# Kernel tuning notes

Measured on AMD Instinct MI355X. Metric: run time of the kernel, lower is better.

Reference implementation:

```python
import jax, jax.numpy as jnp
import numpy as np
from jax import lax

B = 16384
D_MODEL = 84
N_EXPERTS = 2
TOP_K = 2
HIDDEN = 2048


def _conv(x, w, b):
    # x: [N,C,H,W], w: [O,I,kh,kw] (torch OIHW), VALID padding, stride 1
    y = lax.conv_general_dilated(x, w, (1, 1), 'VALID',
                                 dimension_numbers=('NCHW', 'OIHW', 'NCHW'))
    return y + b[None, :, None, None]


def _maxpool2(x):
    return lax.reduce_window(x, -jnp.inf, lax.max,
                             (1, 1, 2, 2), (1, 1, 2, 2), 'VALID')


def setup_inputs() -> dict:
    key = jax.random.key(0)
    ks = jax.random.split(key, 17)
    s = 0.05
    return {
        'x': jax.random.normal(ks[0], (B, 3, 32, 32), jnp.float32),
        'conv1_w': jax.random.normal(ks[1], (6, 3, 5, 5), jnp.float32) * s,
        'conv1_b': jax.random.normal(ks[2], (6,), jnp.float32) * s,
        'conv2_w': jax.random.normal(ks[3], (16, 6, 5, 5), jnp.float32) * s,
        'conv2_b': jax.random.normal(ks[4], (16,), jnp.float32) * s,
        'fc1_w': jax.random.normal(ks[5], (400, 120), jnp.float32) * s,
        'fc1_b': jax.random.normal(ks[6], (120,), jnp.float32) * s,
        'fc2_w': jax.random.normal(ks[7], (120, 84), jnp.float32) * s,
        'fc2_b': jax.random.normal(ks[8], (84,), jnp.float32) * s,
        'gate_w': jax.random.normal(ks[9], (D_MODEL, N_EXPERTS), jnp.float32) * s,
        'exp_w1': jax.random.normal(ks[10], (N_EXPERTS, D_MODEL, HIDDEN), jnp.float32) * s,
        'exp_b1': jax.random.normal(ks[11], (N_EXPERTS, HIDDEN), jnp.float32) * s,
        'exp_w2': jax.random.normal(ks[12], (N_EXPERTS, HIDDEN, D_MODEL), jnp.float32) * s,
        'exp_b2': jax.random.normal(ks[13], (N_EXPERTS, D_MODEL), jnp.float32) * s,
        'fc3_w': jax.random.normal(ks[14], (84, 10), jnp.float32) * s,
        'fc3_b': jax.random.normal(ks[15], (10,), jnp.float32) * s,
    }


def _moe(x, gate_w, exp_w1, exp_b1, exp_w2, exp_b2):
    # tutel top-k gate: softmax over expert logits, select top-k, renormalize
    n = x.shape[0]
    scores = jax.nn.softmax(x @ gate_w, axis=-1)          # [N,E]
    top_v, top_i = lax.top_k(scores, TOP_K)               # [N,k]
    gates = top_v / jnp.sum(top_v, axis=-1, keepdims=True)
    # dense combine weights [N,E] (zero where not routed)
    comb = jnp.zeros((n, N_EXPERTS), x.dtype).at[
        jnp.arange(n)[:, None], top_i].set(gates)
    # grouped expert FFN (E=2: evaluate both, weight-combine)
    h = jax.nn.relu(jnp.einsum('nd,edh->enh', x, exp_w1) + exp_b1[:, None, :])
    y = jnp.einsum('enh,ehd->end', h, exp_w2) + exp_b2[:, None, :]  # [E,N,D]
    return jnp.einsum('ne,end->nd', comb, y)


def reference(x, conv1_w, conv1_b, conv2_w, conv2_b, fc1_w, fc1_b,
              fc2_w, fc2_b, gate_w, exp_w1, exp_b1, exp_w2, exp_b2,
              fc3_w, fc3_b):
    h = _maxpool2(jax.nn.relu(_conv(x, conv1_w, conv1_b)))   # [B,6,14,14]
    h = _maxpool2(jax.nn.relu(_conv(h, conv2_w, conv2_b)))   # [B,16,5,5]
    h = h.reshape(-1, 16 * 5 * 5)                            # [B,400]
    h = jax.nn.relu(h @ fc1_w + fc1_b)                       # [B,120]
    h = jax.nn.relu(h @ fc2_w + fc2_b)                       # [B,84]
    h = _moe(h, gate_w, exp_w1, exp_b1, exp_w2, exp_b2)      # [B,84]
    return h @ fc3_w + fc3_b                                 # [B,10]
```

## Files before the change

kernel.cpp:

```cpp
#include <hip/hip_runtime.h>
#include <stdint.h>

typedef unsigned short u16;
typedef __attribute__((ext_vector_type(8))) short s8v;
typedef __attribute__((ext_vector_type(4))) float f4v;
typedef __fp16 h2v __attribute__((ext_vector_type(2)));
typedef __fp16 h8v __attribute__((ext_vector_type(8)));

__device__ __forceinline__ float bu2f(u16 u) {
  return __uint_as_float(((uint32_t)u) << 16);
}
__device__ __forceinline__ u16 f2bu(float f) {
  uint32_t u = __float_as_uint(f);
  u += 0x7fffu + ((u >> 16) & 1u);
  return (u16)(u >> 16);
}

union U32H2 { uint32_t u; h2v h; };

__device__ __forceinline__ uint32_t pk2h(float a, float b) {
  U32H2 x;
  x.h = __builtin_amdgcn_cvt_pkrtz(a, b);
  return x.u;
}

template <bool F32> struct In;
template <> struct In<true> {
  static __device__ __forceinline__ float ld(const void* p, long i) {
    return ((const float*)p)[i];
  }
};
template <> struct In<false> {
  static __device__ __forceinline__ float ld(const void* p, long i) {
    return bu2f(((const u16*)p)[i]);
  }
};

__global__ void k_detect(const u16* __restrict__ x, int* __restrict__ flag) {
  __shared__ int s[64];
  int cnt = 0;
  for (int i = threadIdx.x; i < 2048; i += 64) {
    int e = (x[i] >> 7) & 0xFF;
    cnt += (e >= 96 && e <= 134) ? 1 : 0;
  }
  s[threadIdx.x] = cnt;
  __syncthreads();
  if (threadIdx.x == 0) {
    int t = 0;
    for (int i = 0; i < 64; ++i) t += s[i];
    *flag = (t >= 1843) ? 0 : 1;
  }
}

__device__ __forceinline__ u16 f2h16(float f) {
  __fp16 h = (__fp16)f;
  u16 r;
  __builtin_memcpy(&r, &h, 2);
  return r;
}

template <bool INF32>
__global__ __launch_bounds__(256) void k_trans(
    const int* __restrict__ flag,
    const void* __restrict__ fc1w, const void* __restrict__ fc2w,
    const void* __restrict__ ew1, const void* __restrict__ ew2,
    const void* __restrict__ c1w, const void* __restrict__ c1b,
    const void* __restrict__ c2w, const void* __restrict__ c2b,
    u16* __restrict__ fc1t, u16* __restrict__ fc2t,
    u16* __restrict__ w1t, u16* __restrict__ w2t,
    uint32_t* __restrict__ cdw) {
  if (*flag != (INF32 ? 1 : 0)) return;
  long gid = (long)blockIdx.x * 256 + threadIdx.x;
  if (gid < 53248) {
    int n = (int)(gid / 416), k = (int)(gid % 416);
    fc1t[gid] = (n < 120 && k < 400) ? f2bu(In<INF32>::ld(fc1w, (long)k * 120 + n)) : (u16)0;
  } else if (gid < 65536) {
    long i = gid - 53248;
    int n = (int)(i / 128), k = (int)(i % 128);
    fc2t[i] = (n < 84 && k < 120) ? f2bu(In<INF32>::ld(fc2w, (long)k * 84 + n)) : (u16)0;
  } else if (gid < 458752) {
    long i = gid - 65536;
    int e = (int)(i / 196608);
    long r = i % 196608;
    int n = (int)(r / 96), k = (int)(r % 96);
    w1t[i] = (k < 84) ? f2bu(In<INF32>::ld(ew1, ((long)e * 84 + k) * 2048 + n)) : (u16)0;
  } else if (gid < 851968) {
    long i = gid - 458752;
    int e = (int)(i / 196608);
    long r = i % 196608;
    int n = (int)(r / 2048), k = (int)(r % 2048);
    w2t[i] = (n < 84) ? f2bu(In<INF32>::ld(ew2, ((long)e * 2048 + k) * 84 + n)) : (u16)0;
  } else if (gid < 856598) {
    long i = gid - 851968;
    u16* cdh = (u16*)cdw;
    if (i < 1536) {
      int ic = (int)(i >> 9);
      int r = (int)(i & 511);
      int lnn = r >> 3, j = r & 7;
      int n = lnn & 15, qd = lnn >> 4;
      int t = qd * 8 + j, ky = t / 6, kxp = t - ky * 6;
      float v = (n < 6 && t < 30 && kxp < 5)
          ? In<INF32>::ld(c1w, ((long)(n * 3 + ic) * 5 + ky) * 5 + kxp) : 0.f;
      cdh[i] = f2h16(v);
    } else if (i < 4608) {
      long jj = i - 1536;
      int ic = (int)(jj >> 9);
      int r = (int)(jj & 511);
      int lnn = r >> 3, j = r & 7;
      int n = lnn & 15, qd = lnn >> 4;
      int t = qd * 8 + j, ky = t / 6, kxp = t - ky * 6;
      float v = (t < 30 && kxp < 5)
          ? In<INF32>::ld(c2w, ((long)(n * 6 + ic) * 5 + ky) * 5 + kxp) : 0.f;
      cdh[1536 + jj] = f2h16(v);
    } else if (i < 4614) {
      ((float*)(cdw + 2304))[i - 4608] = In<INF32>::ld(c1b, i - 4608);
    } else if (i < 4630) {
      ((float*)(cdw + 2310))[i - 4614] = In<INF32>::ld(c2b, i - 4614);
    }
  }
}

#define CIMG 2
#define XSTR 34
#define PSTR 18
#define SXELEMS (CIMG * 3 * 32 * XSTR)
#define SPELEMS (CIMG * 6 * 14 * PSTR)
template <bool INF32>
__global__ __launch_bounds__(256) void k_conv(
    const int* __restrict__ flag,
    const void* __restrict__ x,
    const uint32_t* __restrict__ cdw,
    u16* __restrict__ p2, int Btot) {
  if (*flag != (INF32 ? 1 : 0)) return;
  __shared__ __align__(16) u16 sxbuf[2 * SXELEMS + 16];
  __shared__ __align__(16) u16 sp1buf[2 * SPELEMS + 16];
  __shared__ u16 lut1[196];
  __shared__ u16 lut2[32];
  u16* sxn = sxbuf;
  u16* sxs = sxbuf + SXELEMS + 16;
  u16* sp1n = sp1buf;
  u16* sp1s = sp1buf + SPELEMS + 16;
  const u16* cdh = (const u16*)cdw;
  const float* cb1f = (const float*)(cdw + 2304);
  const float* cb2f = (const float*)(cdw + 2310);
  const int tid = threadIdx.x;
  const int wv = tid >> 6, ln = tid & 63;
  const int mrow = ln & 15, quad = ln >> 4;
  const long gimg0 = (long)blockIdx.x * CIMG;

  if (tid < 196) {
    int py = tid / 14, px = tid - py * 14;
    lut1[tid] = (u16)((2 * py) * XSTR + 2 * px);
  } else if (tid < 228) {
    int i = tid - 196;
    if (i < 25) {
      int py = i / 5, px = i - py * 5;
      lut2[i] = (u16)((2 * py) * PSTR + 2 * px);
    }
  }
  for (int r = tid; r < CIMG * 6 * 14; r += 256)
    *(uint32_t*)(sp1s + (size_t)r * PSTR + 12) = 0;

  for (int i = tid; i < CIMG * 96; i += 256) {
    int img = i / 96;
    if (gimg0 + img >= Btot) continue;
    int rem = i - img * 96;
    long goff = (gimg0 + img) * 3072 + (long)rem * 32;
    uint32_t e[17];
    if (!INF32) {
      const uint32_t* src = (const uint32_t*)((const u16*)x + goff);
#pragma unroll
      for (int j = 0; j < 16; ++j) {
        uint32_t d = src[j];
        e[j] = pk2h(__uint_as_float(d << 16), __uint_as_float(d & 0xffff0000u));
      }
    } else {
      const float* src = (const float*)x + goff;
#pragma unroll
      for (int j = 0; j < 16; ++j) e[j] = pk2h(src[2 * j], src[2 * j + 1]);
    }
    e[16] = 0;
    uint32_t* dn = (uint32_t*)(sxn + (size_t)i * XSTR);
    uint32_t* dsh = (uint32_t*)(sxs + (size_t)i * XSTR);
#pragma unroll
    for (int j = 0; j < 16; ++j) {
      dn[j] = e[j];
      dsh[j] = (e[j] >> 16) | (e[j + 1] << 16);
    }
  }

  h8v b1[3];
#pragma unroll
  for (int ic = 0; ic < 3; ++ic)
    b1[ic] = *(const h8v*)(cdh + ((size_t)ic * 64 + ln) * 8);
  const float bias1 = (mrow < 6) ? cb1f[mrow] : 0.f;
  int toff1[4];
#pragma unroll
  for (int p = 0; p < 4; ++p) {
    int t = quad * 8 + 2 * p;
    if (t >= 30) t = 24;
    toff1[p] = (t / 6) * (XSTR - 6) + t;
  }
  const int qA = mrow >> 2, dyA = (mrow >> 1) & 1, dxA = mrow & 1;

  __syncthreads();

  const u16* c1base = dxA ? sxs : sxn;
  for (int tg = wv; tg < CIMG * 49; tg += 4) {
    int img = tg / 49, tau = tg - img * 49;
    int pqA = tau * 4 + qA;
    const u16* rb0 = c1base + (size_t)img * (3 * 32 * XSTR) + lut1[pqA] + dyA * XSTR;
    f4v acc = {0.f, 0.f, 0.f, 0.f};
#pragma unroll
    for (int ic = 0; ic < 3; ++ic) {
      const u16* rb = rb0 + ic * (32 * XSTR);
      union { uint32_t w[4]; h8v v; } au;
#pragma unroll
      for (int p = 0; p < 4; ++p)
        au.w[p] = *(const uint32_t*)(rb + toff1[p]);
      acc = __builtin_amdgcn_mfma_f32_16x16x32_f16(au.v, b1[ic], acc, 0, 0, 0);
    }
    float v = fmaxf(fmaxf(acc[0], acc[1]), fmaxf(acc[2], acc[3])) + bias1;
    v = fmaxf(v, 0.f);
    if (mrow < 6) {
      int pqC = tau * 4 + quad;
      int py = (pqC * 4682) >> 16, px = pqC - py * 14;
      int rbase = ((img * 6 + mrow) * 14 + py) * PSTR;
      u16 hv = f2h16(v);
      sp1n[rbase + px] = hv;
      sp1s[rbase + (px ? px - 1 : PSTR - 1)] = hv;
    }
  }

  h8v b2[6];
#pragma unroll
  for (int ic = 0; ic < 6; ++ic)
    b2[ic] = *(const h8v*)(cdh + 1536 + ((size_t)ic * 64 + ln) * 8);
  const float bias2 = cb2f[mrow];
  int toff2[4];
#pragma unroll
  for (int p = 0; p < 4; ++p) {
    int t = quad * 8 + 2 * p;
    if (t >= 30) t = 24;
    toff2[p] = (t / 6) * (PSTR - 6) + t;
  }

  __syncthreads();

  const int NP2 = CIMG * 25;
  const u16* c2base = dxA ? sp1s : sp1n;
  for (int t2 = wv; t2 * 4 < NP2; t2 += 4) {
    int PA = t2 * 4 + qA;
    if (PA >= NP2) PA = NP2 - 1;
    int img = (PA * 41) >> 10, pq = PA - img * 25;
    const u16* rb0 = c2base + (size_t)img * (6 * 14 * PSTR) + lut2[pq] + dyA * PSTR;
    f4v acc = {0.f, 0.f, 0.f, 0.f};
#pragma unroll
    for (int ic = 0; ic < 6; ++ic) {
      const u16* rb = rb0 + ic * (14 * PSTR);
      union { uint32_t w[4]; h8v v; } au;
#pragma unroll
      for (int p = 0; p < 4; ++p)
        au.w[p] = *(const uint32_t*)(rb + toff2[p]);
      acc = __builtin_amdgcn_mfma_f32_16x16x32_f16(au.v, b2[ic], acc, 0, 0, 0);
    }
    float v = fmaxf(fmaxf(acc[0], acc[1]), fmaxf(acc[2], acc[3])) + bias2;
    v = fmaxf(v, 0.f);
    int PC = t2 * 4 + quad;
    if (PC < NP2) {
      int imgc = (PC * 41) >> 10, pqc = PC - imgc * 25;
      if (gimg0 + imgc < Btot)
        p2[(gimg0 + imgc) * 416 + mrow * 25 + pqc] = f2bu(v);
    }
  }

  for (int i = tid; i < CIMG * 16; i += 256) {
    int img = i / 16;
    if (gimg0 + img < Btot) p2[(gimg0 + img) * 416 + 400 + (i & 15)] = 0;
  }
}

template <bool INF32>
__global__ __launch_bounds__(256) void k_fcA(
    const int* __restrict__ flag,
    const u16* __restrict__ p2,
    const u16* __restrict__ fc1t, const u16* __restrict__ fc2t,
    const void* __restrict__ fc1b, const void* __restrict__ fc2b,
    const void* __restrict__ gw,
    u16* __restrict__ a2buf, float* __restrict__ scbuf) {
  if (*flag != (INF32 ? 1 : 0)) return;
  __shared__ __align__(16) char smem[62976];
  u16* a2s = (u16*)smem;
  u16* hs = (u16*)(smem + 13312);
  u16* wbuf = (u16*)(smem + 31232);
  u16* xs = (u16*)(smem + 57856);

  const int tid = threadIdx.x;
  const int wv = tid >> 6, ln = tid & 63;
  const int m = ln & 15, quad = ln >> 4;
  const long t0 = (long)blockIdx.x * 64;
  const int row0 = wv * 16 + quad * 4;

  for (int i = tid; i < 30720 / 4; i += 256) ((uint32_t*)smem)[i] = 0;

  f4v acc1[8];
#pragma unroll
  for (int i = 0; i < 8; ++i) acc1[i] = (f4v){0.f, 0.f, 0.f, 0.f};
  for (int s = 0; s < 13; ++s) {
    {
      int r = tid >> 2, c0 = (tid & 3) * 8;
      *(uint4*)(xs + r * 40 + c0) =
          *(const uint4*)(p2 + (t0 + r) * 416 + s * 32 + c0);
      int n = tid >> 1, cw = (tid & 1) * 16;
      *(uint4*)(wbuf + n * 40 + cw) = *(const uint4*)(fc1t + (long)n * 416 + s * 32 + cw);
      *(uint4*)(wbuf + n * 40 + cw + 8) =
          *(const uint4*)(fc1t + (long)n * 416 + s * 32 + cw + 8);
    }
    __syncthreads();
    s8v a = *(const s8v*)(xs + (wv * 16 + m) * 40 + quad * 8);
#pragma unroll
    for (int nt = 0; nt < 8; ++nt) {
      s8v b = *(const s8v*)(wbuf + (nt * 16 + m) * 40 + quad * 8);
      acc1[nt] = __builtin_amdgcn_mfma_f32_16x16x32_bf16(a, b, acc1[nt], 0, 0, 0);
    }
    __syncthreads();
  }
#pragma unroll
  for (int nt = 0; nt < 8; ++nt) {
    int n = nt * 16 + m;
    if (n < 120) {
      float bv = In<INF32>::ld(fc1b, n);
#pragma unroll
      for (int r = 0; r < 4; ++r)
        hs[(row0 + r) * 136 + n] = f2bu(fmaxf(acc1[nt][r] + bv, 0.f));
    }
  }
  __syncthreads();

  for (int i = tid; i < 1536; i += 256) {
    int n = i >> 4, c0 = (i & 15) * 8;
    *(uint4*)(wbuf + n * 136 + c0) = *(const uint4*)(fc2t + n * 128 + c0);
  }
  __syncthreads();
  f4v acc2[6];
#pragma unroll
  for (int i = 0; i < 6; ++i) acc2[i] = (f4v){0.f, 0.f, 0.f, 0.f};
  for (int s = 0; s < 4; ++s) {
    s8v a = *(const s8v*)(hs + (wv * 16 + m) * 136 + s * 32 + quad * 8);
#pragma unroll
    for (int nt = 0; nt < 6; ++nt) {
      s8v b = *(const s8v*)(wbuf + (nt * 16 + m) * 136 + s * 32 + quad * 8);
      acc2[nt] = __builtin_amdgcn_mfma_f32_16x16x32_bf16(a, b, acc2[nt], 0, 0, 0);
    }
  }
  __syncthreads();
#pragma unroll
  for (int nt = 0; nt < 6; ++nt) {
    int n = nt * 16 + m;
    if (n < 84) {
      float bv = In<INF32>::ld(fc2b, n);
#pragma unroll
      for (int r = 0; r < 4; ++r)
        a2s[(row0 + r) * 104 + n] = f2bu(fmaxf(acc2[nt][r] + bv, 0.f));
    }
  }
  __syncthreads();

  if (tid < 64) {
    const u16* xr = a2s + tid * 104;
    float l0 = 0.f, l1 = 0.f;
    for (int k = 0; k < 84; ++k) {
      float xv = bu2f(xr[k]);
      l0 = fmaf(xv, In<INF32>::ld(gw, 2 * k), l0);
      l1 = fmaf(xv, In<INF32>::ld(gw, 2 * k + 1), l1);
    }
    float mx = fmaxf(l0, l1);
    float e0 = __expf(l0 - mx), e1 = __expf(l1 - mx);
    float inv = 1.f / (e0 + e1);
    *(float2*)(scbuf + (t0 + tid) * 2) = make_float2(e0 * inv, e1 * inv);
  }
  for (int i = tid; i < 832; i += 256) {
    int r = i / 13, c0 = (i - r * 13) * 8;
    *(uint4*)(a2buf + (t0 + r) * 104 + c0) = *(const uint4*)(a2s + r * 104 + c0);
  }
}

template <bool INF32>
__global__ __launch_bounds__(256) void k_exp(
    const int* __restrict__ flag,
    const u16* __restrict__ a2buf, const float* __restrict__ scbuf,
    const u16* __restrict__ w1t, const u16* __restrict__ w2t,
    const void* __restrict__ eb1, const void* __restrict__ eb2,
    float* __restrict__ ybuf, int Btok) {
  if (*flag != (INF32 ? 1 : 0)) return;
  __shared__ __align__(16) char smem[57856];
  u16* a2s = (u16*)smem;
  u16* hs = (u16*)(smem + 13312);
  u16* wbuf = (u16*)(smem + 30720);
  float* scs = (float*)(smem + 57344);

  const int tid = threadIdx.x;
  const int wv = tid >> 6, ln = tid & 63;
  const int m = ln & 15, quad = ln >> 4;
  const int e = blockIdx.y;
  const long t0 = (long)blockIdx.x * 64;
  const int row0 = wv * 16 + quad * 4;
  const u16* w1te = w1t + (long)e * 196608;
  const u16* w2te = w2t + (long)e * 196608;

  for (int i = tid; i < 832; i += 256) {
    int r = i / 13, c0 = (i - r * 13) * 8;
    *(uint4*)(a2s + r * 104 + c0) = *(const uint4*)(a2buf + (t0 + r) * 104 + c0);
  }
  if (tid < 64) scs[tid] = scbuf[(t0 + tid) * 2 + e];
  __syncthreads();

  f4v acce[6];
#pragma unroll
  for (int i = 0; i < 6; ++i) acce[i] = (f4v){0.f, 0.f, 0.f, 0.f};
  for (int c = 0; c < 16; ++c) {
    const int n0 = c * 128;
    if (c) __syncthreads();
    for (int i = tid; i < 1536; i += 256) {
      int nl = i / 12, c0 = (i - nl * 12) * 8;
      *(uint4*)(wbuf + nl * 104 + c0) =
          *(const uint4*)(w1te + (long)(n0 + nl) * 96 + c0);
    }
    __syncthreads();
    f4v acch[8];
#pragma unroll
    for (int i = 0; i < 8; ++i) acch[i] = (f4v){0.f, 0.f, 0.f, 0.f};
    for (int s = 0; s < 3; ++s) {
      s8v a = *(const s8v*)(a2s + (wv * 16 + m) * 104 + s * 32 + quad * 8);
#pragma unroll
      for (int nt = 0; nt < 8; ++nt) {
        s8v b = *(const s8v*)(wbuf + (nt * 16 + m) * 104 + s * 32 + quad * 8);
        acch[nt] = __builtin_amdgcn_mfma_f32_16x16x32_bf16(a, b, acch[nt], 0, 0, 0);
      }
    }
#pragma unroll
    for (int nt = 0; nt < 8; ++nt) {
      float bv = In<INF32>::ld(eb1, (long)e * 2048 + n0 + nt * 16 + m);
#pragma unroll
      for (int r = 0; r < 4; ++r)
        hs[(row0 + r) * 136 + nt * 16 + m] = f2bu(fmaxf(acch[nt][r] + bv, 0.f));
    }
    __syncthreads();
    for (int i = tid; i < 1536; i += 256) {
      int n = i >> 4, c0 = (i & 15) * 8;
      *(uint4*)(wbuf + n * 136 + c0) =
          *(const uint4*)(w2te + (long)n * 2048 + n0 + c0);
    }
    __syncthreads();
    for (int s = 0; s < 4; ++s) {
      s8v a = *(const s8v*)(hs + (wv * 16 + m) * 136 + s * 32 + quad * 8);
#pragma unroll
      for (int nt = 0; nt < 6; ++nt) {
        s8v b = *(const s8v*)(wbuf + (nt * 16 + m) * 136 + s * 32 + quad * 8);
        acce[nt] = __builtin_amdgcn_mfma_f32_16x16x32_bf16(a, b, acce[nt], 0, 0, 0);
      }
    }
  }

#pragma unroll
  for (int nt = 0; nt < 6; ++nt) {
    int d = nt * 16 + m;
    float bv = (d < 84) ? In<INF32>::ld(eb2, (long)e * 84 + d) : 0.f;
#pragma unroll
    for (int r = 0; r < 4; ++r) {
      float sc = scs[row0 + r];
      ybuf[((size_t)e * Btok + t0 + row0 + r) * 96 + d] = sc * (acce[nt][r] + bv);
    }
  }
}

template <bool INF32>
__global__ __launch_bounds__(256) void k_fc3(
    const int* __restrict__ flag,
    const float* __restrict__ ybuf,
    const void* __restrict__ w3, const void* __restrict__ b3,
    void* __restrict__ out, int Btok) {
  if (*flag != (INF32 ? 1 : 0)) return;
  __shared__ float sw3[840];
  __shared__ float sb3[10];
  const int tid = threadIdx.x;
  const long t0 = (long)blockIdx.x * 64;
  for (int i = tid; i < 840; i += 256) sw3[i] = In<INF32>::ld(w3, i);
  if (tid < 10) sb3[tid] = In<INF32>::ld(b3, tid);
  __syncthreads();
  for (int idx = tid; idx < 640; idx += 256) {
    int tk = idx / 10, cc = idx - tk * 10;
    const float* y0r = ybuf + (t0 + tk) * 96;
    const float* y1r = ybuf + ((size_t)Btok + t0 + tk) * 96;
    float acc = sb3[cc];
    for (int d = 0; d < 84; ++d)
      acc = fmaf(y0r[d] + y1r[d], sw3[d * 10 + cc], acc);
    long oi = (t0 + tk) * 10 + cc;
    if (INF32) ((float*)out)[oi] = acc;
    else ((u16*)out)[oi] = f2bu(acc);
  }
}

extern "C" void kernel_launch(void* const* d_in, const int* in_sizes, int n_in,
                              void* d_out, int out_size, void* d_ws, size_t ws_size,
                              hipStream_t stream) {
  const int B = in_sizes[0] / 3072;
  char* wsb = (char*)d_ws;
  int* flag = (int*)wsb;
  u16* p2 = (u16*)(wsb + 64);
  u16* fc1t = p2 + (size_t)B * 416;
  u16* fc2t = fc1t + 53248;
  u16* w1t = fc2t + 12288;
  u16* w2t = w1t + 393216;
  uint32_t* cdw = (uint32_t*)(w2t + 393216);
  u16* a2buf = (u16*)(cdw + 2326);
  float* scbuf = (float*)(a2buf + (size_t)B * 104);
  float* ybuf = scbuf + (size_t)B * 2;

  k_detect<<<1, 64, 0, stream>>>((const u16*)d_in[0], flag);

  k_trans<false><<<3347, 256, 0, stream>>>(flag, d_in[5], d_in[7], d_in[10],
                                           d_in[12], d_in[1], d_in[2], d_in[3],
                                           d_in[4], fc1t, fc2t, w1t, w2t, cdw);
  k_trans<true><<<3347, 256, 0, stream>>>(flag, d_in[5], d_in[7], d_in[10],
                                          d_in[12], d_in[1], d_in[2], d_in[3],
                                          d_in[4], fc1t, fc2t, w1t, w2t, cdw);

  const int convGrid = (B + CIMG - 1) / CIMG;
  k_conv<false><<<convGrid, 256, 0, stream>>>(flag, d_in[0], cdw, p2, B);
  k_conv<true><<<convGrid, 256, 0, stream>>>(flag, d_in[0], cdw, p2, B);

  k_fcA<false><<<B / 64, 256, 0, stream>>>(flag, p2, fc1t, fc2t, d_in[6],
                                           d_in[8], d_in[9], a2buf, scbuf);
  k_fcA<true><<<B / 64, 256, 0, stream>>>(flag, p2, fc1t, fc2t, d_in[6],
                                          d_in[8], d_in[9], a2buf, scbuf);

  dim3 eg(B / 64, 2);
  k_exp<false><<<eg, 256, 0, stream>>>(flag, a2buf, scbuf, w1t, w2t, d_in[11],
                                       d_in[13], ybuf, B);
  k_exp<true><<<eg, 256, 0, stream>>>(flag, a2buf, scbuf, w1t, w2t, d_in[11],
                                      d_in[13], ybuf, B);

  k_fc3<false><<<B / 64, 256, 0, stream>>>(flag, ybuf, d_in[14], d_in[15],
                                           d_out, B);
  k_fc3<true><<<B / 64, 256, 0, stream>>>(flag, ybuf, d_in[14], d_in[15],
                                          d_out, B);
}
```

Before: 499.8 us.

## Vectorize conv input loads, simplify LDS indexing, and restructure fc3 one-token-per-thread

The conv input staging now reads global memory with 16-byte vector loads instead of 4-byte scalar loads. Shared-buffer indexing uses integer offsets from one base, and the division by 49 and 25 is replaced with incremental or compare-based image selection. fc3 is rewritten so each thread owns one token and computes all 10 outputs with float4 reads of the expert outputs, launching a quarter as many blocks. The fc3 change trades per-thread parallelism for register reuse and fewer redundant reads, and it assumes the token count is a multiple of 256.

Result: no change. 497.1 us (-0.5%).

```diff
diff --git a/kernel.cpp b/kernel.cpp
--- a/kernel.cpp
+++ b/kernel.cpp
@@ -125,6 +125,8 @@
 #define PSTR 18
 #define SXELEMS (CIMG * 3 * 32 * XSTR)
 #define SPELEMS (CIMG * 6 * 14 * PSTR)
+#define SXSHIFT (SXELEMS + 16)
+#define SPSHIFT (SPELEMS + 16)
 template <bool INF32>
 __global__ __launch_bounds__(256) void k_conv(
     const int* __restrict__ flag,
@@ -136,10 +138,6 @@
   __shared__ __align__(16) u16 sp1buf[2 * SPELEMS + 16];
   __shared__ u16 lut1[196];
   __shared__ u16 lut2[32];
-  u16* sxn = sxbuf;
-  u16* sxs = sxbuf + SXELEMS + 16;
-  u16* sp1n = sp1buf;
-  u16* sp1s = sp1buf + SPELEMS + 16;
   const u16* cdh = (const u16*)cdw;
   const float* cb1f = (const float*)(cdw + 2304);
   const float* cb2f = (const float*)(cdw + 2310);
@@ -159,29 +157,37 @@
     }
   }
   for (int r = tid; r < CIMG * 6 * 14; r += 256)
-    *(uint32_t*)(sp1s + (size_t)r * PSTR + 12) = 0;
+    *(uint32_t*)(sp1buf + SPSHIFT + r * PSTR + 12) = 0;
 
   for (int i = tid; i < CIMG * 96; i += 256) {
-    int img = i / 96;
+    int img = (i >= 96) ? 1 : 0;
     if (gimg0 + img >= Btot) continue;
     int rem = i - img * 96;
     long goff = (gimg0 + img) * 3072 + (long)rem * 32;
     uint32_t e[17];
     if (!INF32) {
-      const uint32_t* src = (const uint32_t*)((const u16*)x + goff);
-#pragma unroll
-      for (int j = 0; j < 16; ++j) {
-        uint32_t d = src[j];
-        e[j] = pk2h(__uint_as_float(d << 16), __uint_as_float(d & 0xffff0000u));
+      const uint4* src = (const uint4*)((const u16*)x + goff);
+#pragma unroll
+      for (int j = 0; j < 4; ++j) {
+        uint4 d = src[j];
+        e[4 * j + 0] = pk2h(__uint_as_float(d.x << 16), __uint_as_float(d.x & 0xffff0000u));
+        e[4 * j + 1] = pk2h(__uint_as_float(d.y << 16), __uint_as_float(d.y & 0xffff0000u));
+        e[4 * j + 2] = pk2h(__uint_as_float(d.z << 16), __uint_as_float(d.z & 0xffff0000u));
+        e[4 * j + 3] = pk2h(__uint_as_float(d.w << 16), __uint_as_float(d.w & 0xffff0000u));
       }
     } else {
-      const float* src = (const float*)x + goff;
-#pragma unroll
-      for (int j = 0; j < 16; ++j) e[j] = pk2h(src[2 * j], src[2 * j + 1]);
+      const float4* src = (const float4*)((const float*)x + goff);
+#pragma unroll
+      for (int j = 0; j < 8; ++j) {
+        float4 v = src[j];
+        e[2 * j] = pk2h(v.x, v.y);
+        e[2 * j + 1] = pk2h(v.z, v.w);
+      }
     }
     e[16] = 0;
-    uint32_t* dn = (uint32_t*)(sxn + (size_t)i * XSTR);
-    uint32_t* dsh = (uint32_t*)(sxs + (size_t)i * XSTR);
+    const int b = i * XSTR;
+    uint32_t* dn = (uint32_t*)(sxbuf + b);
+    uint32_t* dsh = (uint32_t*)(sxbuf + SXSHIFT + b);
 #pragma unroll
     for (int j = 0; j < 16; ++j) {
       dn[j] = e[j];
@@ -192,7 +198,7 @@
   h8v b1[3];
 #pragma unroll
   for (int ic = 0; ic < 3; ++ic)
-    b1[ic] = *(const h8v*)(cdh + ((size_t)ic * 64 + ln) * 8);
+    b1[ic] = *(const h8v*)(cdh + ic * 512 + ln * 8);
   const float bias1 = (mrow < 6) ? cb1f[mrow] : 0.f;
   int toff1[4];
 #pragma unroll
@@ -205,37 +211,41 @@
 
   __syncthreads();
 
-  const u16* c1base = dxA ? sxs : sxn;
-  for (int tg = wv; tg < CIMG * 49; tg += 4) {
-    int img = tg / 49, tau = tg - img * 49;
-    int pqA = tau * 4 + qA;
-    const u16* rb0 = c1base + (size_t)img * (3 * 32 * XSTR) + lut1[pqA] + dyA * XSTR;
-    f4v acc = {0.f, 0.f, 0.f, 0.f};
-#pragma unroll
-    for (int ic = 0; ic < 3; ++ic) {
-      const u16* rb = rb0 + ic * (32 * XSTR);
-      union { uint32_t w[4]; h8v v; } au;
-#pragma unroll
-      for (int p = 0; p < 4; ++p)
-        au.w[p] = *(const uint32_t*)(rb + toff1[p]);
-      acc = __builtin_amdgcn_mfma_f32_16x16x32_f16(au.v, b1[ic], acc, 0, 0, 0);
-    }
-    float v = fmaxf(fmaxf(acc[0], acc[1]), fmaxf(acc[2], acc[3])) + bias1;
-    v = fmaxf(v, 0.f);
-    if (mrow < 6) {
-      int pqC = tau * 4 + quad;
-      int py = (pqC * 4682) >> 16, px = pqC - py * 14;
-      int rbase = ((img * 6 + mrow) * 14 + py) * PSTR;
-      u16 hv = f2h16(v);
-      sp1n[rbase + px] = hv;
-      sp1s[rbase + (px ? px - 1 : PSTR - 1)] = hv;
+  {
+    const int c1off = dxA ? SXSHIFT : 0;
+    int img = 0, tau = wv;
+    for (int tg = wv; tg < CIMG * 49; tg += 4) {
+      int pqA = tau * 4 + qA;
+      int rb0 = c1off + img * (3 * 32 * XSTR) + lut1[pqA] + dyA * XSTR;
+      f4v acc = {0.f, 0.f, 0.f, 0.f};
+#pragma unroll
+      for (int ic = 0; ic < 3; ++ic) {
+        int rb = rb0 + ic * (32 * XSTR);
+        union { uint32_t w[4]; h8v v; } au;
+#pragma unroll
+        for (int p = 0; p < 4; ++p)
+          au.w[p] = *(const uint32_t*)(sxbuf + rb + toff1[p]);
+        acc = __builtin_amdgcn_mfma_f32_16x16x32_f16(au.v, b1[ic], acc, 0, 0, 0);
+      }
+      float v = fmaxf(fmaxf(acc[0], acc[1]), fmaxf(acc[2], acc[3])) + bias1;
+      v = fmaxf(v, 0.f);
+      if (mrow < 6) {
+        int pqC = tau * 4 + quad;
+        int py = (pqC * 4682) >> 16, px = pqC - py * 14;
+        int rbase = ((img * 6 + mrow) * 14 + py) * PSTR;
+        u16 hv = f2h16(v);
+        sp1buf[rbase + px] = hv;
+        sp1buf[SPSHIFT + rbase + (px ? px - 1 : PSTR - 1)] = hv;
+      }
+      tau += 4;
+      if (tau >= 49) { tau -= 49; ++img; }
     }
   }
 
   h8v b2[6];
 #pragma unroll
   for (int ic = 0; ic < 6; ++ic)
-    b2[ic] = *(const h8v*)(cdh + 1536 + ((size_t)ic * 64 + ln) * 8);
+    b2[ic] = *(const h8v*)(cdh + 1536 + ic * 512 + ln * 8);
   const float bias2 = cb2f[mrow];
   int toff2[4];
 #pragma unroll
@@ -247,30 +257,34 @@
 
   __syncthreads();
 
-  const int NP2 = CIMG * 25;
-  const u16* c2base = dxA ? sp1s : sp1n;
-  for (int t2 = wv; t2 * 4 < NP2; t2 += 4) {
-    int PA = t2 * 4 + qA;
-    if (PA >= NP2) PA = NP2 - 1;
-    int img = (PA * 41) >> 10, pq = PA - img * 25;
-    const u16* rb0 = c2base + (size_t)img * (6 * 14 * PSTR) + lut2[pq] + dyA * PSTR;
-    f4v acc = {0.f, 0.f, 0.f, 0.f};
-#pragma unroll
-    for (int ic = 0; ic < 6; ++ic) {
-      const u16* rb = rb0 + ic * (14 * PSTR);
-      union { uint32_t w[4]; h8v v; } au;
-#pragma unroll
-      for (int p = 0; p < 4; ++p)
-        au.w[p] = *(const uint32_t*)(rb + toff2[p]);
-      acc = __builtin_amdgcn_mfma_f32_16x16x32_f16(au.v, b2[ic], acc, 0, 0, 0);
-    }
-    float v = fmaxf(fmaxf(acc[0], acc[1]), fmaxf(acc[2], acc[3])) + bias2;
-    v = fmaxf(v, 0.f);
-    int PC = t2 * 4 + quad;
-    if (PC < NP2) {
-      int imgc = (PC * 41) >> 10, pqc = PC - imgc * 25;
-      if (gimg0 + imgc < Btot)
-        p2[(gimg0 + imgc) * 416 + mrow * 25 + pqc] = f2bu(v);
+  {
+    const int NP2 = CIMG * 25;
+    const int c2off = dxA ? SPSHIFT : 0;
+    for (int t2 = wv; t2 * 4 < NP2; t2 += 4) {
+      int PA = t2 * 4 + qA;
+      if (PA >= NP2) PA = NP2 - 1;
+      int img2 = (PA >= 25) ? 1 : 0;
+      int pq = PA - img2 * 25;
+      int rb0 = c2off + img2 * (6 * 14 * PSTR) + lut2[pq] + dyA * PSTR;
+      f4v acc = {0.f, 0.f, 0.f, 0.f};
+#pragma unroll
+      for (int ic = 0; ic < 6; ++ic) {
+        int rb = rb0 + ic * (14 * PSTR);
+        union { uint32_t w[4]; h8v v; } au;
+#pragma unroll
+        for (int p = 0; p < 4; ++p)
+          au.w[p] = *(const uint32_t*)(sp1buf + rb + toff2[p]);
+        acc = __builtin_amdgcn_mfma_f32_16x16x32_f16(au.v, b2[ic], acc, 0, 0, 0);
+      }
+      float v = fmaxf(fmaxf(acc[0], acc[1]), fmaxf(acc[2], acc[3])) + bias2;
+      v = fmaxf(v, 0.f);
+      int PC = t2 * 4 + quad;
+      if (PC < NP2) {
+        int imgc = (PC >= 25) ? 1 : 0;
+        int pqc = PC - imgc * 25;
+        if (gimg0 + imgc < Btot)
+          p2[(gimg0 + imgc) * 416 + mrow * 25 + pqc] = f2bu(v);
+      }
     }
   }
 
@@ -484,20 +498,34 @@
   __shared__ float sw3[840];
   __shared__ float sb3[10];
   const int tid = threadIdx.x;
-  const long t0 = (long)blockIdx.x * 64;
   for (int i = tid; i < 840; i += 256) sw3[i] = In<INF32>::ld(w3, i);
   if (tid < 10) sb3[tid] = In<INF32>::ld(b3, tid);
   __syncthreads();
-  for (int idx = tid; idx < 640; idx += 256) {
-    int tk = idx / 10, cc = idx - tk * 10;
-    const float* y0r = ybuf + (t0 + tk) * 96;
-    const float* y1r = ybuf + ((size_t)Btok + t0 + tk) * 96;
-    float acc = sb3[cc];
-    for (int d = 0; d < 84; ++d)
-      acc = fmaf(y0r[d] + y1r[d], sw3[d * 10 + cc], acc);
-    long oi = (t0 + tk) * 10 + cc;
-    if (INF32) ((float*)out)[oi] = acc;
-    else ((u16*)out)[oi] = f2bu(acc);
+  const long tk = (long)blockIdx.x * 256 + tid;
+  const float4* y0r = (const float4*)(ybuf + tk * 96);
+  const float4* y1r = (const float4*)(ybuf + ((size_t)Btok + tk) * 96);
+  float o[10];
+#pragma unroll
+  for (int c = 0; c < 10; ++c) o[c] = sb3[c];
+#pragma unroll
+  for (int d4 = 0; d4 < 21; ++d4) {
+    float4 a = y0r[d4], b = y1r[d4];
+    float s0 = a.x + b.x, s1 = a.y + b.y, s2 = a.z + b.z, s3 = a.w + b.w;
+    const float* w = sw3 + d4 * 40;
+#pragma unroll
+    for (int c = 0; c < 10; ++c)
+      o[c] = fmaf(s0, w[c],
+             fmaf(s1, w[10 + c],
+             fmaf(s2, w[20 + c],
+             fmaf(s3, w[30 + c], o[c]))));
+  }
+  long oi = tk * 10;
+  if (INF32) {
+#pragma unroll
+    for (int c = 0; c < 10; ++c) ((float*)out)[oi + c] = o[c];
+  } else {
+#pragma unroll
+    for (int c = 0; c < 10; ++c) ((u16*)out)[oi + c] = f2bu(o[c]);
   }
 }
 
@@ -541,8 +569,8 @@
   k_exp<true><<<eg, 256, 0, stream>>>(flag, a2buf, scbuf, w1t, w2t, d_in[11],
                                       d_in[13], ybuf, B);
 
-  k_fc3<false><<<B / 64, 256, 0, stream>>>(flag, ybuf, d_in[14], d_in[15],
+  k_fc3<false><<<B / 256, 256, 0, stream>>>(flag, ybuf, d_in[14], d_in[15],
+                                            d_out, B);
+  k_fc3<true><<<B / 256, 256, 0, stream>>>(flag, ybuf, d_in[14], d_in[15],
                                            d_out, B);
-  k_fc3<true><<<B / 64, 256, 0, stream>>>(flag, ybuf, d_in[14], d_in[15],
-                                          d_out, B);
-}
+}
```
